# Performance work log

Hardware: AMD Instinct MI355X
Metric: run time of the kernel (lower is better)

## Reference

```python
import jax, jax.numpy as jnp
import numpy as np

N_NODES = 100000
N_EDGES = 1600000
D = 64
K = 10


def setup_inputs() -> dict:
    key = jax.random.key(0)
    k1, k2, k3, k4 = jax.random.split(key, 4)
    features = jax.random.normal(k1, (N_NODES, D), dtype=jnp.float32)
    s = jax.random.normal(k2, (D, 1), dtype=jnp.float32)
    src = jax.random.randint(k3, (N_EDGES,), 0, N_NODES, dtype=jnp.int64)
    dst = jax.random.randint(k4, (N_EDGES,), 0, N_NODES, dtype=jnp.int64)
    return {"features": features, "s": s, "src": src, "dst": dst, "k": K}


def reference(features, s, src, dst, k):
    n = features.shape[0]
    # symmetric degree norm: deg_in clamped at 1, norm = deg^{-1/2}
    deg = jax.ops.segment_sum(jnp.ones_like(dst, dtype=features.dtype), dst,
                              num_segments=n)
    norm = jnp.power(jnp.maximum(deg, 1.0), -0.5)[:, None]  # [N,1]

    def step(h, _):
        h = h * norm
        # copy_u + sum: scatter-add src features into dst nodes (SpMM)
        h = jax.ops.segment_sum(h[src], dst, num_segments=n)
        h = h * norm
        return h, h

    _, hops = jax.lax.scan(step, features, None, length=k)  # [k,N,D]
    H = jnp.concatenate([features[None], hops], axis=0)      # [k+1,N,D]
    H = jnp.transpose(H, (1, 0, 2))                           # [N,k+1,D]
    # attention pooling: S = sigmoid(H @ s), out = S^T H
    S = jax.nn.sigmoid(jnp.einsum('nkd,d->nk', H, s[:, 0]))  # [N,k+1]
    out = jnp.einsum('nk,nkd->nd', S, H)                      # [N,D]
    return out
```

## Files before the change

kernel.cpp:

```cpp
#include <hip/hip_runtime.h>
#include <math.h>

#define D 64
#define RB 1024
#define EB 2048
#define NRMAX 128


__device__ __forceinline__ float4 f4scale(float4 a, float b) {
    return make_float4(a.x * b, a.y * b, a.z * b, a.w * b);
}

__device__ __forceinline__ unsigned int bf16_rne(float x) {
    unsigned int u = __float_as_uint(x);
    u += 0x7fffu + ((u >> 16) & 1u);
    return u >> 16;
}

__device__ __forceinline__ uint4 pack_bf16x8(const float* v) {
    uint4 p;
    p.x = bf16_rne(v[0]) | (bf16_rne(v[1]) << 16);
    p.y = bf16_rne(v[2]) | (bf16_rne(v[3]) << 16);
    p.z = bf16_rne(v[4]) | (bf16_rne(v[5]) << 16);
    p.w = bf16_rne(v[6]) | (bf16_rne(v[7]) << 16);
    return p;
}

__device__ __forceinline__ void acc_bf16x8(uint4 p, float* a) {
    a[0] += __uint_as_float(p.x << 16);
    a[1] += __uint_as_float(p.x & 0xffff0000u);
    a[2] += __uint_as_float(p.y << 16);
    a[3] += __uint_as_float(p.y & 0xffff0000u);
    a[4] += __uint_as_float(p.z << 16);
    a[5] += __uint_as_float(p.z & 0xffff0000u);
    a[6] += __uint_as_float(p.w << 16);
    a[7] += __uint_as_float(p.w & 0xffff0000u);
}


__global__ void countA(const int* __restrict__ dst, int* __restrict__ countsA_T,
                       int E, int NR, int NBLK) {
    __shared__ int hist[NRMAX];
    int t = threadIdx.x;
    for (int i = t; i < NR; i += 256) hist[i] = 0;
    __syncthreads();
    int base = blockIdx.x * EB + t;
    #pragma unroll
    for (int j = 0; j < EB / 256; ++j) {
        int e = base + j * 256;
        if (e < E) atomicAdd(&hist[dst[e] >> 10], 1);
    }
    __syncthreads();
    for (int i = t; i < NR; i += 256) countsA_T[i * NBLK + blockIdx.x] = hist[i];
}

__global__ void block_sums(const int* __restrict__ arr, int* __restrict__ bsum, int n) {
    int base = blockIdx.x * 1024;
    int t = threadIdx.x;
    int v = 0;
    #pragma unroll
    for (int j = 0; j < 4; ++j) {
        int i = base + t + j * 256;
        if (i < n) v += arr[i];
    }
    #pragma unroll
    for (int m = 32; m >= 1; m >>= 1) v += __shfl_xor(v, m, 64);
    __shared__ int ws[4];
    if ((t & 63) == 0) ws[t >> 6] = v;
    __syncthreads();
    if (t == 0) bsum[blockIdx.x] = ws[0] + ws[1] + ws[2] + ws[3];
}

__global__ void scan_bsums(int* __restrict__ bsum, int nb) {
    __shared__ int tmp[1024];
    int t = threadIdx.x;
    int v = (t < nb) ? bsum[t] : 0;
    tmp[t] = v;
    __syncthreads();
    for (int off = 1; off < 1024; off <<= 1) {
        int x = (t >= off) ? tmp[t - off] : 0;
        __syncthreads();
        tmp[t] += x;
        __syncthreads();
    }
    if (t < nb) bsum[t] = tmp[t] - v;
}

__global__ void gen_scan2(const int* __restrict__ arr, const int* __restrict__ bsum,
                          int* __restrict__ out, int n) {
    __shared__ int tmp[1024];
    int base = blockIdx.x * 1024;
    int t = threadIdx.x;
    int i = base + t;
    int v = (i < n) ? arr[i] : 0;
    tmp[t] = v;
    __syncthreads();
    for (int off = 1; off < 1024; off <<= 1) {
        int x = (t >= off) ? tmp[t - off] : 0;
        __syncthreads();
        tmp[t] += x;
        __syncthreads();
    }
    if (i < n) out[i] = bsum[blockIdx.x] + tmp[t] - v;
}

__global__ void passA2(const int* __restrict__ src, const int* __restrict__ dst,
                       const int* __restrict__ baseA, unsigned int* __restrict__ ebuf2,
                       int E, int NR, int NBLK) {
    __shared__ int cur[NRMAX];
    int t = threadIdx.x;
    for (int i = t; i < NR; i += 256) cur[i] = baseA[i * NBLK + blockIdx.x];
    __syncthreads();
    int base = blockIdx.x * EB + t;
    #pragma unroll
    for (int j = 0; j < EB / 256; ++j) {
        int e = base + j * 256;
        if (e < E) {
            int v = dst[e];
            int pos = atomicAdd(&cur[v >> 10], 1);
            ebuf2[pos] = (unsigned int)src[e] | ((unsigned int)(v & (RB - 1)) << 17);
        }
    }
}

__global__ void range_build(const unsigned int* __restrict__ ebuf2,
                            const int* __restrict__ baseA,
                            int* __restrict__ offsets, float* __restrict__ norm,
                            int* __restrict__ csr, int N, int E, int NR, int NBLK) {
    __shared__ int cnt[RB];
    __shared__ int sc[RB];
    int rg = blockIdx.x;
    int t = threadIdx.x;
    int r0 = baseA[rg * NBLK];
    int r1 = (rg + 1 < NR) ? baseA[(rg + 1) * NBLK] : E;
    cnt[t] = 0;
    __syncthreads();
    for (int i = r0 + t; i < r1; i += RB)
        atomicAdd(&cnt[ebuf2[i] >> 17], 1);
    __syncthreads();
    int v = cnt[t];
    sc[t] = v;
    __syncthreads();
    for (int off = 1; off < RB; off <<= 1) {
        int x = (t >= off) ? sc[t - off] : 0;
        __syncthreads();
        sc[t] += x;
        __syncthreads();
    }
    int excl = sc[t] - v;
    int node = rg * RB + t;
    if (node < N) {
        offsets[node] = r0 + excl;
        norm[node] = rsqrtf((float)(v > 1 ? v : 1));
    }
    if (rg == NR - 1 && t == 0) offsets[N] = E;
    __syncthreads();
    cnt[t] = r0 + excl;
    __syncthreads();
    for (int i = r0 + t; i < r1; i += RB) {
        unsigned int u = ebuf2[i];
        int pos = atomicAdd(&cnt[u >> 17], 1);
        csr[pos] = (int)(u & 0x1FFFFu);
    }
}


__global__ void hop0(const float4* __restrict__ feat, const float* __restrict__ s,
                     const float* __restrict__ norm, uint4* __restrict__ g,
                     float4* __restrict__ out, int n) {
    int t = blockIdx.x * blockDim.x + threadIdx.x;
    int node = t >> 3;
    int l = t & 7;
    if (node >= n) return;
    float4 f0 = feat[node * 16 + 2 * l];
    float4 f1 = feat[node * 16 + 2 * l + 1];
    const float4* s4 = (const float4*)s;
    float4 a = s4[2 * l], b = s4[2 * l + 1];
    float dot = f0.x * a.x + f0.y * a.y + f0.z * a.z + f0.w * a.w
              + f1.x * b.x + f1.y * b.y + f1.z * b.z + f1.w * b.w;
    #pragma unroll
    for (int m = 1; m <= 4; m <<= 1) dot += __shfl_xor(dot, m, 64);
    float sig = 1.0f / (1.0f + expf(-dot));
    out[node * 16 + 2 * l]     = f4scale(f0, sig);
    out[node * 16 + 2 * l + 1] = f4scale(f1, sig);
    float nv = norm[node];
    float v[8] = {f0.x * nv, f0.y * nv, f0.z * nv, f0.w * nv,
                  f1.x * nv, f1.y * nv, f1.z * nv, f1.w * nv};
    g[node * 8 + l] = pack_bf16x8(v);
}


__global__ void spmm_hop(const uint4* __restrict__ gin, const int* __restrict__ offsets,
                         const int* __restrict__ csr, const float* __restrict__ norm,
                         const float* __restrict__ s, uint4* __restrict__ gout,
                         float4* __restrict__ out, int n) {
    int lane = threadIdx.x & 63;
    int node = blockIdx.x * 4 + (threadIdx.x >> 6);
    if (node >= n) return;
    int g = lane >> 3;
    int l = lane & 7;
    int beg = offsets[node], end = offsets[node + 1];
    int deg = end - beg;
    int dcap = deg < 64 ? deg : 64;
    int idx = (lane < dcap) ? csr[beg + lane] : 0;

    float acc[8] = {0.f, 0.f, 0.f, 0.f, 0.f, 0.f, 0.f, 0.f};
    {
        int e0 = g, e1 = g + 8, e2 = g + 16, e3 = g + 24;
        int u0 = __shfl(idx, e0, 64);
        int u1 = __shfl(idx, e1, 64);
        int u2 = __shfl(idx, e2, 64);
        int u3 = __shfl(idx, e3, 64);
        uint4 p0 = gin[(size_t)u0 * 8 + l];
        uint4 p1 = gin[(size_t)u1 * 8 + l];
        uint4 p2 = gin[(size_t)u2 * 8 + l];
        uint4 p3 = gin[(size_t)u3 * 8 + l];
        if (e0 < dcap) acc_bf16x8(p0, acc);
        if (e1 < dcap) acc_bf16x8(p1, acc);
        if (e2 < dcap) acc_bf16x8(p2, acc);
        if (e3 < dcap) acc_bf16x8(p3, acc);
    }
    if (dcap > 32) {
        int e0 = g + 32, e1 = g + 40, e2 = g + 48, e3 = g + 56;
        int u0 = __shfl(idx, e0, 64);
        int u1 = __shfl(idx, e1, 64);
        int u2 = __shfl(idx, e2, 64);
        int u3 = __shfl(idx, e3, 64);
        uint4 p0 = gin[(size_t)u0 * 8 + l];
        uint4 p1 = gin[(size_t)u1 * 8 + l];
        uint4 p2 = gin[(size_t)u2 * 8 + l];
        uint4 p3 = gin[(size_t)u3 * 8 + l];
        if (e0 < dcap) acc_bf16x8(p0, acc);
        if (e1 < dcap) acc_bf16x8(p1, acc);
        if (e2 < dcap) acc_bf16x8(p2, acc);
        if (e3 < dcap) acc_bf16x8(p3, acc);
    }
    for (int i = beg + 64 + g; i < end; i += 8) {
        acc_bf16x8(gin[(size_t)csr[i] * 8 + l], acc);
    }

    #pragma unroll
    for (int m = 8; m <= 32; m <<= 1) {
        #pragma unroll
        for (int jj = 0; jj < 8; ++jj) acc[jj] += __shfl_xor(acc[jj], m, 64);
    }

    float nv = norm[node];
    float h[8];
    #pragma unroll
    for (int jj = 0; jj < 8; ++jj) h[jj] = acc[jj] * nv;

    const float4* s4 = (const float4*)s;
    float4 a = s4[2 * l], b = s4[2 * l + 1];
    float dot = h[0] * a.x + h[1] * a.y + h[2] * a.z + h[3] * a.w
              + h[4] * b.x + h[5] * b.y + h[6] * b.z + h[7] * b.w;
    #pragma unroll
    for (int m = 1; m <= 4; m <<= 1) dot += __shfl_xor(dot, m, 64);
    float sig = 1.0f / (1.0f + expf(-dot));

    if (g == 0) {
        float gv[8];
        #pragma unroll
        for (int jj = 0; jj < 8; ++jj) gv[jj] = h[jj] * nv;
        gout[node * 8 + l] = pack_bf16x8(gv);
        float4 o0 = out[node * 16 + 2 * l];
        float4 o1 = out[node * 16 + 2 * l + 1];
        o0.x += sig * h[0]; o0.y += sig * h[1]; o0.z += sig * h[2]; o0.w += sig * h[3];
        o1.x += sig * h[4]; o1.y += sig * h[5]; o1.z += sig * h[6]; o1.w += sig * h[7];
        out[node * 16 + 2 * l]     = o0;
        out[node * 16 + 2 * l + 1] = o1;
    }
}


extern "C" void kernel_launch(void* const* d_in, const int* in_sizes, int n_in,
                              void* d_out, int out_size, void* d_ws, size_t ws_size,
                              hipStream_t stream) {
    const float* feat = (const float*)d_in[0];
    const float* s    = (const float*)d_in[1];
    const int*   src  = (const int*)d_in[2];
    const int*   dst  = (const int*)d_in[3];
    const int K = 10;

    int N = in_sizes[0] / D;
    int E = in_sizes[2];
    int NR   = (N + RB - 1) / RB;
    int NBLK = (E + EB - 1) / EB;
    int M    = NR * NBLK;
    int nchA = (M + 1023) / 1024;

    int*   offsets  = (int*)d_ws;
    int*   csr      = offsets + (N + 1);
    float* norm     = (float*)(csr + E);
    int*   countsA  = (int*)(norm + N);
    int*   baseA    = countsA + M;
    int*   bsumA    = baseA + M;
    uintptr_t p = (uintptr_t)(bsumA + nchA);
    p = (p + 255) & ~(uintptr_t)255;
    uint4* g0 = (uint4*)p;
    uint4* g1 = g0 + (size_t)N * 8;
    unsigned int* ebuf2 = (unsigned int*)g1;

    countA<<<NBLK, 256, 0, stream>>>(dst, countsA, E, NR, NBLK);
    block_sums<<<nchA, 256, 0, stream>>>(countsA, bsumA, M);
    scan_bsums<<<1, 1024, 0, stream>>>(bsumA, nchA);
    gen_scan2<<<nchA, 1024, 0, stream>>>(countsA, bsumA, baseA, M);
    passA2<<<NBLK, 256, 0, stream>>>(src, dst, baseA, ebuf2, E, NR, NBLK);
    range_build<<<NR, RB, 0, stream>>>(ebuf2, baseA, offsets, norm, csr, N, E, NR, NBLK);

    hop0<<<(N * 8 + 255) / 256, 256, 0, stream>>>(
        (const float4*)feat, s, norm, g0, (float4*)d_out, N);

    uint4* gin = g0; uint4* gout = g1;
    for (int t = 0; t < K; ++t) {
        spmm_hop<<<(N + 3) / 4, 256, 0, stream>>>(
            gin, offsets, csr, norm, s, gout, (float4*)d_out, N);
        uint4* tmp = gin; gin = gout; gout = tmp;
    }
}
```

Measured before the change: 576.8 us.

## Switch gather buffers to fp16 with half2 accumulation and defer attention pooling

Replaces the bf16 gather buffers with fp16 and accumulates the first 64 neighbours with packed __hadd2 instead of unpacking to fp32. When the workspace is large enough, every hop's normalized features are kept and a single epilogue kernel does the sigmoid-attention pooling, so each hop no longer read-modify-writes the fp32 output. The last hop in the fallback path also skips writing its unused g buffer. Summing in fp16 and recovering h by dividing by norm can lose precision or overflow at high degree, and the deferred path needs eleven N×64 half buffers of workspace.

```diff
diff --git a/kernel.cpp b/kernel.cpp
--- a/kernel.cpp
+++ b/kernel.cpp
@@ -1,41 +1,15 @@
 #include <hip/hip_runtime.h>
+#include <hip/hip_fp16.h>
 #include <math.h>
 
 #define D 64
 #define RB 1024
 #define EB 2048
 #define NRMAX 128
-
-
-__device__ __forceinline__ float4 f4scale(float4 a, float b) {
-    return make_float4(a.x * b, a.y * b, a.z * b, a.w * b);
-}
-
-__device__ __forceinline__ unsigned int bf16_rne(float x) {
-    unsigned int u = __float_as_uint(x);
-    u += 0x7fffu + ((u >> 16) & 1u);
-    return u >> 16;
-}
-
-__device__ __forceinline__ uint4 pack_bf16x8(const float* v) {
-    uint4 p;
-    p.x = bf16_rne(v[0]) | (bf16_rne(v[1]) << 16);
-    p.y = bf16_rne(v[2]) | (bf16_rne(v[3]) << 16);
-    p.z = bf16_rne(v[4]) | (bf16_rne(v[5]) << 16);
-    p.w = bf16_rne(v[6]) | (bf16_rne(v[7]) << 16);
-    return p;
-}
-
-__device__ __forceinline__ void acc_bf16x8(uint4 p, float* a) {
-    a[0] += __uint_as_float(p.x << 16);
-    a[1] += __uint_as_float(p.x & 0xffff0000u);
-    a[2] += __uint_as_float(p.y << 16);
-    a[3] += __uint_as_float(p.y & 0xffff0000u);
-    a[4] += __uint_as_float(p.z << 16);
-    a[5] += __uint_as_float(p.z & 0xffff0000u);
-    a[6] += __uint_as_float(p.w << 16);
-    a[7] += __uint_as_float(p.w & 0xffff0000u);
-}
+#define KHOPS 10
+
+
+typedef union { uint4 u; __half2 h[4]; } U4H;
 
 
 __global__ void countA(const int* __restrict__ dst, int* __restrict__ countsA_T,
@@ -166,34 +140,39 @@
 
 
 __global__ void hop0(const float4* __restrict__ feat, const float* __restrict__ s,
-                     const float* __restrict__ norm, uint4* __restrict__ g,
-                     float4* __restrict__ out, int n) {
+                     const float* __restrict__ norm, uint4* __restrict__ g0,
+                     float4* __restrict__ out, int n, int do_pool) {
     int t = blockIdx.x * blockDim.x + threadIdx.x;
     int node = t >> 3;
     int l = t & 7;
     if (node >= n) return;
     float4 f0 = feat[node * 16 + 2 * l];
     float4 f1 = feat[node * 16 + 2 * l + 1];
-    const float4* s4 = (const float4*)s;
-    float4 a = s4[2 * l], b = s4[2 * l + 1];
-    float dot = f0.x * a.x + f0.y * a.y + f0.z * a.z + f0.w * a.w
-              + f1.x * b.x + f1.y * b.y + f1.z * b.z + f1.w * b.w;
-    #pragma unroll
-    for (int m = 1; m <= 4; m <<= 1) dot += __shfl_xor(dot, m, 64);
-    float sig = 1.0f / (1.0f + expf(-dot));
-    out[node * 16 + 2 * l]     = f4scale(f0, sig);
-    out[node * 16 + 2 * l + 1] = f4scale(f1, sig);
     float nv = norm[node];
-    float v[8] = {f0.x * nv, f0.y * nv, f0.z * nv, f0.w * nv,
-                  f1.x * nv, f1.y * nv, f1.z * nv, f1.w * nv};
-    g[node * 8 + l] = pack_bf16x8(v);
+    U4H P;
+    P.h[0] = __floats2half2_rn(f0.x * nv, f0.y * nv);
+    P.h[1] = __floats2half2_rn(f0.z * nv, f0.w * nv);
+    P.h[2] = __floats2half2_rn(f1.x * nv, f1.y * nv);
+    P.h[3] = __floats2half2_rn(f1.z * nv, f1.w * nv);
+    g0[node * 8 + l] = P.u;
+    if (do_pool) {
+        const float4* s4 = (const float4*)s;
+        float4 a = s4[2 * l], b = s4[2 * l + 1];
+        float dot = f0.x * a.x + f0.y * a.y + f0.z * a.z + f0.w * a.w
+                  + f1.x * b.x + f1.y * b.y + f1.z * b.z + f1.w * b.w;
+        #pragma unroll
+        for (int m = 1; m <= 4; m <<= 1) dot += __shfl_xor(dot, m, 64);
+        float sig = 1.0f / (1.0f + expf(-dot));
+        out[node * 16 + 2 * l]     = make_float4(sig * f0.x, sig * f0.y, sig * f0.z, sig * f0.w);
+        out[node * 16 + 2 * l + 1] = make_float4(sig * f1.x, sig * f1.y, sig * f1.z, sig * f1.w);
+    }
 }
 
 
 __global__ void spmm_hop(const uint4* __restrict__ gin, const int* __restrict__ offsets,
                          const int* __restrict__ csr, const float* __restrict__ norm,
                          const float* __restrict__ s, uint4* __restrict__ gout,
-                         float4* __restrict__ out, int n) {
+                         float4* __restrict__ out, int n, int do_pool, int write_g) {
     int lane = threadIdx.x & 63;
     int node = blockIdx.x * 4 + (threadIdx.x >> 6);
     if (node >= n) return;
@@ -204,21 +183,23 @@
     int dcap = deg < 64 ? deg : 64;
     int idx = (lane < dcap) ? csr[beg + lane] : 0;
 
-    float acc[8] = {0.f, 0.f, 0.f, 0.f, 0.f, 0.f, 0.f, 0.f};
+    __half2 z = __floats2half2_rn(0.f, 0.f);
+    __half2 ah0 = z, ah1 = z, ah2 = z, ah3 = z;
     {
         int e0 = g, e1 = g + 8, e2 = g + 16, e3 = g + 24;
         int u0 = __shfl(idx, e0, 64);
         int u1 = __shfl(idx, e1, 64);
         int u2 = __shfl(idx, e2, 64);
         int u3 = __shfl(idx, e3, 64);
-        uint4 p0 = gin[(size_t)u0 * 8 + l];
-        uint4 p1 = gin[(size_t)u1 * 8 + l];
-        uint4 p2 = gin[(size_t)u2 * 8 + l];
-        uint4 p3 = gin[(size_t)u3 * 8 + l];
-        if (e0 < dcap) acc_bf16x8(p0, acc);
-        if (e1 < dcap) acc_bf16x8(p1, acc);
-        if (e2 < dcap) acc_bf16x8(p2, acc);
-        if (e3 < dcap) acc_bf16x8(p3, acc);
+        U4H A, B, C, Dd;
+        A.u = gin[(size_t)u0 * 8 + l];
+        B.u = gin[(size_t)u1 * 8 + l];
+        C.u = gin[(size_t)u2 * 8 + l];
+        Dd.u = gin[(size_t)u3 * 8 + l];
+        if (e0 < dcap) { ah0 = __hadd2(ah0, A.h[0]); ah1 = __hadd2(ah1, A.h[1]); ah2 = __hadd2(ah2, A.h[2]); ah3 = __hadd2(ah3, A.h[3]); }
+        if (e1 < dcap) { ah0 = __hadd2(ah0, B.h[0]); ah1 = __hadd2(ah1, B.h[1]); ah2 = __hadd2(ah2, B.h[2]); ah3 = __hadd2(ah3, B.h[3]); }
+        if (e2 < dcap) { ah0 = __hadd2(ah0, C.h[0]); ah1 = __hadd2(ah1, C.h[1]); ah2 = __hadd2(ah2, C.h[2]); ah3 = __hadd2(ah3, C.h[3]); }
+        if (e3 < dcap) { ah0 = __hadd2(ah0, Dd.h[0]); ah1 = __hadd2(ah1, Dd.h[1]); ah2 = __hadd2(ah2, Dd.h[2]); ah3 = __hadd2(ah3, Dd.h[3]); }
     }
     if (dcap > 32) {
         int e0 = g + 32, e1 = g + 40, e2 = g + 48, e3 = g + 56;
@@ -226,17 +207,27 @@
         int u1 = __shfl(idx, e1, 64);
         int u2 = __shfl(idx, e2, 64);
         int u3 = __shfl(idx, e3, 64);
-        uint4 p0 = gin[(size_t)u0 * 8 + l];
-        uint4 p1 = gin[(size_t)u1 * 8 + l];
-        uint4 p2 = gin[(size_t)u2 * 8 + l];
-        uint4 p3 = gin[(size_t)u3 * 8 + l];
-        if (e0 < dcap) acc_bf16x8(p0, acc);
-        if (e1 < dcap) acc_bf16x8(p1, acc);
-        if (e2 < dcap) acc_bf16x8(p2, acc);
-        if (e3 < dcap) acc_bf16x8(p3, acc);
-    }
+        U4H A, B, C, Dd;
+        A.u = gin[(size_t)u0 * 8 + l];
+        B.u = gin[(size_t)u1 * 8 + l];
+        C.u = gin[(size_t)u2 * 8 + l];
+        Dd.u = gin[(size_t)u3 * 8 + l];
+        if (e0 < dcap) { ah0 = __hadd2(ah0, A.h[0]); ah1 = __hadd2(ah1, A.h[1]); ah2 = __hadd2(ah2, A.h[2]); ah3 = __hadd2(ah3, A.h[3]); }
+        if (e1 < dcap) { ah0 = __hadd2(ah0, B.h[0]); ah1 = __hadd2(ah1, B.h[1]); ah2 = __hadd2(ah2, B.h[2]); ah3 = __hadd2(ah3, B.h[3]); }
+        if (e2 < dcap) { ah0 = __hadd2(ah0, C.h[0]); ah1 = __hadd2(ah1, C.h[1]); ah2 = __hadd2(ah2, C.h[2]); ah3 = __hadd2(ah3, C.h[3]); }
+        if (e3 < dcap) { ah0 = __hadd2(ah0, Dd.h[0]); ah1 = __hadd2(ah1, Dd.h[1]); ah2 = __hadd2(ah2, Dd.h[2]); ah3 = __hadd2(ah3, Dd.h[3]); }
+    }
+
+    float2 q0 = __half22float2(ah0), q1 = __half22float2(ah1);
+    float2 q2 = __half22float2(ah2), q3 = __half22float2(ah3);
+    float acc[8] = {q0.x, q0.y, q1.x, q1.y, q2.x, q2.y, q3.x, q3.y};
+
     for (int i = beg + 64 + g; i < end; i += 8) {
-        acc_bf16x8(gin[(size_t)csr[i] * 8 + l], acc);
+        U4H P; P.u = gin[(size_t)csr[i] * 8 + l];
+        float2 a0 = __half22float2(P.h[0]), a1 = __half22float2(P.h[1]);
+        float2 a2 = __half22float2(P.h[2]), a3 = __half22float2(P.h[3]);
+        acc[0] += a0.x; acc[1] += a0.y; acc[2] += a1.x; acc[3] += a1.y;
+        acc[4] += a2.x; acc[5] += a2.y; acc[6] += a3.x; acc[7] += a3.y;
     }
 
     #pragma unroll
@@ -250,26 +241,66 @@
     #pragma unroll
     for (int jj = 0; jj < 8; ++jj) h[jj] = acc[jj] * nv;
 
+    float sig = 0.f;
+    if (do_pool) {
+        const float4* s4 = (const float4*)s;
+        float4 a = s4[2 * l], b = s4[2 * l + 1];
+        float dot = h[0] * a.x + h[1] * a.y + h[2] * a.z + h[3] * a.w
+                  + h[4] * b.x + h[5] * b.y + h[6] * b.z + h[7] * b.w;
+        #pragma unroll
+        for (int m = 1; m <= 4; m <<= 1) dot += __shfl_xor(dot, m, 64);
+        sig = 1.0f / (1.0f + expf(-dot));
+    }
+
+    if (g == 0) {
+        if (write_g) {
+            U4H P;
+            P.h[0] = __floats2half2_rn(h[0] * nv, h[1] * nv);
+            P.h[1] = __floats2half2_rn(h[2] * nv, h[3] * nv);
+            P.h[2] = __floats2half2_rn(h[4] * nv, h[5] * nv);
+            P.h[3] = __floats2half2_rn(h[6] * nv, h[7] * nv);
+            gout[node * 8 + l] = P.u;
+        }
+        if (do_pool) {
+            float4 o0 = out[node * 16 + 2 * l];
+            float4 o1 = out[node * 16 + 2 * l + 1];
+            o0.x += sig * h[0]; o0.y += sig * h[1]; o0.z += sig * h[2]; o0.w += sig * h[3];
+            o1.x += sig * h[4]; o1.y += sig * h[5]; o1.z += sig * h[6]; o1.w += sig * h[7];
+            out[node * 16 + 2 * l]     = o0;
+            out[node * 16 + 2 * l + 1] = o1;
+        }
+    }
+}
+
+
+__global__ void pool_epilogue(const uint4* __restrict__ gbase, size_t gstride,
+                              const float* __restrict__ norm,
+                              const float* __restrict__ s,
+                              float4* __restrict__ out, int N) {
+    int t0 = blockIdx.x * blockDim.x + threadIdx.x;
+    int node = t0 >> 3;
+    int l = t0 & 7;
+    if (node >= N) return;
+    float inv_nv = 1.0f / norm[node];
     const float4* s4 = (const float4*)s;
-    float4 a = s4[2 * l], b = s4[2 * l + 1];
-    float dot = h[0] * a.x + h[1] * a.y + h[2] * a.z + h[3] * a.w
-              + h[4] * b.x + h[5] * b.y + h[6] * b.z + h[7] * b.w;
-    #pragma unroll
-    for (int m = 1; m <= 4; m <<= 1) dot += __shfl_xor(dot, m, 64);
-    float sig = 1.0f / (1.0f + expf(-dot));
-
-    if (g == 0) {
-        float gv[8];
-        #pragma unroll
-        for (int jj = 0; jj < 8; ++jj) gv[jj] = h[jj] * nv;
-        gout[node * 8 + l] = pack_bf16x8(gv);
-        float4 o0 = out[node * 16 + 2 * l];
-        float4 o1 = out[node * 16 + 2 * l + 1];
-        o0.x += sig * h[0]; o0.y += sig * h[1]; o0.z += sig * h[2]; o0.w += sig * h[3];
-        o1.x += sig * h[4]; o1.y += sig * h[5]; o1.z += sig * h[6]; o1.w += sig * h[7];
-        out[node * 16 + 2 * l]     = o0;
-        out[node * 16 + 2 * l + 1] = o1;
-    }
+    float4 sa = s4[2 * l], sb = s4[2 * l + 1];
+    float o[8] = {0.f, 0.f, 0.f, 0.f, 0.f, 0.f, 0.f, 0.f};
+    for (int t = 0; t <= KHOPS; ++t) {
+        U4H P; P.u = gbase[(size_t)t * gstride + (size_t)node * 8 + l];
+        float2 a0 = __half22float2(P.h[0]), a1 = __half22float2(P.h[1]);
+        float2 a2 = __half22float2(P.h[2]), a3 = __half22float2(P.h[3]);
+        float gf[8] = {a0.x, a0.y, a1.x, a1.y, a2.x, a2.y, a3.x, a3.y};
+        float dot = gf[0] * sa.x + gf[1] * sa.y + gf[2] * sa.z + gf[3] * sa.w
+                  + gf[4] * sb.x + gf[5] * sb.y + gf[6] * sb.z + gf[7] * sb.w;
+        #pragma unroll
+        for (int m = 1; m <= 4; m <<= 1) dot += __shfl_xor(dot, m, 64);
+        float sig = 1.0f / (1.0f + expf(-dot * inv_nv));
+        float sc = sig * inv_nv;
+        #pragma unroll
+        for (int j = 0; j < 8; ++j) o[j] += sc * gf[j];
+    }
+    out[node * 16 + 2 * l]     = make_float4(o[0], o[1], o[2], o[3]);
+    out[node * 16 + 2 * l + 1] = make_float4(o[4], o[5], o[6], o[7]);
 }
 
 
@@ -280,7 +311,6 @@
     const float* s    = (const float*)d_in[1];
     const int*   src  = (const int*)d_in[2];
     const int*   dst  = (const int*)d_in[3];
-    const int K = 10;
 
     int N = in_sizes[0] / D;
     int E = in_sizes[2];
@@ -297,9 +327,13 @@
     int*   bsumA    = baseA + M;
     uintptr_t p = (uintptr_t)(bsumA + nchA);
     p = (p + 255) & ~(uintptr_t)255;
-    uint4* g0 = (uint4*)p;
-    uint4* g1 = g0 + (size_t)N * 8;
-    unsigned int* ebuf2 = (unsigned int*)g1;
+    uint4* gbase = (uint4*)p;
+    size_t gstride = (size_t)N * 8;
+
+    size_t fixed_bytes = (uintptr_t)gbase - (uintptr_t)d_ws;
+    int deferred = (ws_size >= fixed_bytes + (size_t)(KHOPS + 1) * gstride * sizeof(uint4)) ? 1 : 0;
+
+    unsigned int* ebuf2 = (unsigned int*)(gbase + gstride);
 
     countA<<<NBLK, 256, 0, stream>>>(dst, countsA, E, NR, NBLK);
     block_sums<<<nchA, 256, 0, stream>>>(countsA, bsumA, M);
@@ -308,13 +342,27 @@
     passA2<<<NBLK, 256, 0, stream>>>(src, dst, baseA, ebuf2, E, NR, NBLK);
     range_build<<<NR, RB, 0, stream>>>(ebuf2, baseA, offsets, norm, csr, N, E, NR, NBLK);
 
-    hop0<<<(N * 8 + 255) / 256, 256, 0, stream>>>(
-        (const float4*)feat, s, norm, g0, (float4*)d_out, N);
-
-    uint4* gin = g0; uint4* gout = g1;
-    for (int t = 0; t < K; ++t) {
-        spmm_hop<<<(N + 3) / 4, 256, 0, stream>>>(
-            gin, offsets, csr, norm, s, gout, (float4*)d_out, N);
-        uint4* tmp = gin; gin = gout; gout = tmp;
-    }
-}
+    float4* outp = (float4*)d_out;
+    int nb_node8 = (N * 8 + 255) / 256;
+    int nb_spmm  = (N + 3) / 4;
+
+    hop0<<<nb_node8, 256, 0, stream>>>((const float4*)feat, s, norm, gbase,
+                                       outp, N, deferred ? 0 : 1);
+
+    if (deferred) {
+        for (int t = 0; t < KHOPS; ++t) {
+            spmm_hop<<<nb_spmm, 256, 0, stream>>>(
+                gbase + (size_t)t * gstride, offsets, csr, norm, s,
+                gbase + (size_t)(t + 1) * gstride, outp, N, 0, 1);
+        }
+        pool_epilogue<<<nb_node8, 256, 0, stream>>>(gbase, gstride, norm, s, outp, N);
+    } else {
+        uint4* gin = gbase;
+        uint4* gout = gbase + gstride;
+        for (int t = 0; t < KHOPS; ++t) {
+            spmm_hop<<<nb_spmm, 256, 0, stream>>>(
+                gin, offsets, csr, norm, s, gout, outp, N, 1, (t < KHOPS - 1) ? 1 : 0);
+            uint4* tmp = gin; gin = gout; gout = tmp;
+        }
+    }
+}
```

New measurement: 526.7 us. -8.7%, faster.
